# Optimization experiments

Measured on AMD Instinct MI355X. Metric: run time of the kernel, lower is better.

## Reference

```python
import jax, jax.numpy as jnp
import numpy as np

N, E, F_IN, F_HID, K = 100000, 1600000, 64, 64, 6


def setup_inputs() -> dict:
    key = jax.random.key(0)
    k1, k2, k3, k4, k5 = jax.random.split(key, 5)
    x = jax.random.normal(k1, (N, F_IN), dtype=jnp.float32)
    # edges with no self-loops (PyG ChebConv removes self loops before normalization)
    src = jax.random.randint(k2, (E,), 0, N, dtype=jnp.int32)
    off = jax.random.randint(k3, (E,), 1, N, dtype=jnp.int32)
    dst = (src + off) % N
    edge_index = jnp.stack([src, dst], axis=0)
    # Glorot-ish init for the K Chebyshev weight matrices
    W = jax.random.normal(k4, (K, F_IN, F_HID), dtype=jnp.float32) * (1.0 / np.sqrt(F_IN))
    b = jax.random.normal(k5, (F_HID,), dtype=jnp.float32) * 0.01
    return {"x": x, "edge_index": edge_index, "W": W, "b": b}


def reference(x, edge_index, W, b):
    # ChebConv with sym normalization, lambda_max = 2.0 (PyG default):
    # scaled Laplacian L_hat = 2*L/lambda_max - I = -D^{-1/2} A D^{-1/2} (zero diagonal)
    row = edge_index[0].astype(jnp.int32)  # source j
    col = edge_index[1].astype(jnp.int32)  # target i
    n = x.shape[0]
    deg = jax.ops.segment_sum(jnp.ones_like(row, dtype=x.dtype), row, num_segments=n)
    dinv = jnp.where(deg > 0, jax.lax.rsqrt(deg), jnp.zeros_like(deg))
    w = -(dinv[row] * dinv[col])  # [E] edge weights of L_hat

    def prop(h):  # h: [N, F] -> L_hat @ h via gather-scale-scatter
        return jax.ops.segment_sum(w[:, None] * h[row], col, num_segments=n)

    # Chebyshev recurrence: Tx_0 = x, Tx_1 = L_hat x, Tx_k = 2 L_hat Tx_{k-1} - Tx_{k-2}
    Tx0 = x
    out = Tx0 @ W[0]
    Tx1 = prop(Tx0)
    out = out + Tx1 @ W[1]
    for k in range(2, W.shape[0]):
        Tx2 = 2.0 * prop(Tx1) - Tx0
        out = out + Tx2 @ W[k]
        Tx0, Tx1 = Tx1, Tx2
    return jax.nn.relu(out + b)
```

## Files before the change

### kernel.cpp

```cpp
#include <hip/hip_runtime.h>


constexpr int F = 64;
constexpr int SCAN_ELEMS = 2048;
constexpr int BSH = 9;
constexpr int EPB = 2048;
constexpr int PNPW = 8;
constexpr int WFRAG_BLOCKS = 12;

typedef __attribute__((ext_vector_type(8))) short short8;
typedef __attribute__((ext_vector_type(4))) float floatx4;

__device__ __forceinline__ unsigned short f_to_bf(float f) {
    unsigned u = __float_as_uint(f);
    u += 0x7FFFu + ((u >> 16) & 1u);
    return (unsigned short)(u >> 16);
}
__device__ __forceinline__ float bf_to_f(unsigned short s) {
    return __uint_as_float(((unsigned)s) << 16);
}
__device__ __forceinline__ float4 bf4_to_f4(ushort4 u) {
    float4 f;
    f.x = bf_to_f(u.x); f.y = bf_to_f(u.y); f.z = bf_to_f(u.z); f.w = bf_to_f(u.w);
    return f;
}

__global__ void hist2_kernel(const int* __restrict__ row, const int* __restrict__ col,
                             int* __restrict__ gcH, int* __restrict__ gcS,
                             int P, int G, int E) {
    __shared__ int hH[256], hS[256];
    const int tid = threadIdx.x, blk = blockIdx.x;
    hH[tid] = 0; hS[tid] = 0;
    __syncthreads();
    const int start = blk * EPB + tid * 8;
    if (start + 7 < E) {
        const int4 c0 = *(const int4*)(col + start);
        const int4 c1 = *(const int4*)(col + start + 4);
        const int4 r0 = *(const int4*)(row + start);
        const int4 r1 = *(const int4*)(row + start + 4);
        atomicAdd(&hH[c0.x >> BSH], 1); atomicAdd(&hH[c0.y >> BSH], 1);
        atomicAdd(&hH[c0.z >> BSH], 1); atomicAdd(&hH[c0.w >> BSH], 1);
        atomicAdd(&hH[c1.x >> BSH], 1); atomicAdd(&hH[c1.y >> BSH], 1);
        atomicAdd(&hH[c1.z >> BSH], 1); atomicAdd(&hH[c1.w >> BSH], 1);
        atomicAdd(&hS[r0.x >> BSH], 1); atomicAdd(&hS[r0.y >> BSH], 1);
        atomicAdd(&hS[r0.z >> BSH], 1); atomicAdd(&hS[r0.w >> BSH], 1);
        atomicAdd(&hS[r1.x >> BSH], 1); atomicAdd(&hS[r1.y >> BSH], 1);
        atomicAdd(&hS[r1.z >> BSH], 1); atomicAdd(&hS[r1.w >> BSH], 1);
    } else {
        for (int k = start; k < E && k < start + 8; ++k) {
            atomicAdd(&hH[col[k] >> BSH], 1);
            atomicAdd(&hS[row[k] >> BSH], 1);
        }
    }
    __syncthreads();
    if (tid < P) {
        gcH[(size_t)tid * G + blk] = hH[tid];
        gcS[(size_t)tid * G + blk] = hS[tid];
    }
}

__device__ __forceinline__ int4 load_cnt4(const int* __restrict__ cnt, int i, int N) {
    int4 v = make_int4(0, 0, 0, 0);
    if (i + 3 < N) {
        v = *(const int4*)(cnt + i);
    } else {
        if (i + 0 < N) v.x = cnt[i + 0];
        if (i + 1 < N) v.y = cnt[i + 1];
        if (i + 2 < N) v.z = cnt[i + 2];
        if (i + 3 < N) v.w = cnt[i + 3];
    }
    return v;
}

__global__ void scan1_kernel(const int* __restrict__ cnt, int* __restrict__ bsum, int N) {
    const int tid = threadIdx.x;
    const int i = blockIdx.x * SCAN_ELEMS + tid * 8;
    int4 va = load_cnt4(cnt, i, N);
    int4 vb = load_cnt4(cnt, i + 4, N);
    int s = va.x + va.y + va.z + va.w + vb.x + vb.y + vb.z + vb.w;
#pragma unroll
    for (int off = 1; off < 64; off <<= 1) s += __shfl_xor(s, off);
    __shared__ int ws[4];
    if ((tid & 63) == 0) ws[tid >> 6] = s;
    __syncthreads();
    if (tid == 0) bsum[blockIdx.x] = ws[0] + ws[1] + ws[2] + ws[3];
}

__global__ void scan3_kernel(const int* __restrict__ cnt, const int* __restrict__ bsum,
                             int* __restrict__ dst, int N) {
    const int tid = threadIdx.x;
    const int lane = tid & 63, w = tid >> 6;
    const int blk = blockIdx.x;
    __shared__ int wsum[4];
    __shared__ int boffs;
    {
        int a = 0;
        for (int k = tid; k < blk; k += 256) a += bsum[k];
#pragma unroll
        for (int off = 1; off < 64; off <<= 1) a += __shfl_xor(a, off);
        if ((tid & 63) == 0) wsum[tid >> 6] = a;
        __syncthreads();
        if (tid == 0) boffs = wsum[0] + wsum[1] + wsum[2] + wsum[3];
        __syncthreads();
    }
    const int i = blk * SCAN_ELEMS + tid * 8;
    int4 va = load_cnt4(cnt, i, N);
    int4 vb = load_cnt4(cnt, i + 4, N);
    const int s = va.x + va.y + va.z + va.w + vb.x + vb.y + vb.z + vb.w;
    int inc = s;
#pragma unroll
    for (int off = 1; off < 64; off <<= 1) {
        int t = __shfl_up(inc, off);
        if (lane >= off) inc += t;
    }
    __syncthreads();
    if (lane == 63) wsum[w] = inc;
    __syncthreads();
    int wo = 0;
    for (int k = 0; k < w; ++k) wo += wsum[k];
    const int r0 = boffs + wo + inc - s;
    const int r1 = r0 + va.x, r2 = r1 + va.y, r3 = r2 + va.z;
    const int r4 = r3 + va.w, r5 = r4 + vb.x, r6 = r5 + vb.y, r7 = r6 + vb.z;
    if (i + 3 < N) {
        *(int4*)(dst + i) = make_int4(r0, r1, r2, r3);
    } else {
        if (i + 0 < N) dst[i + 0] = r0;
        if (i + 1 < N) dst[i + 1] = r1;
        if (i + 2 < N) dst[i + 2] = r2;
    }
    if (i + 7 < N) {
        *(int4*)(dst + i + 4) = make_int4(r4, r5, r6, r7);
    } else {
        if (i + 4 < N) dst[i + 4] = r4;
        if (i + 5 < N) dst[i + 5] = r5;
        if (i + 6 < N) dst[i + 6] = r6;
    }
}

__global__ void part2_kernel(const int* __restrict__ row, const int* __restrict__ col,
                             const int* __restrict__ goH, const int* __restrict__ goS,
                             int* __restrict__ partH, unsigned short* __restrict__ partS,
                             int P, int G, int E) {
    __shared__ int cH[256], cS[256];
    const int tid = threadIdx.x, blk = blockIdx.x;
    if (tid < P) {
        cH[tid] = goH[(size_t)tid * G + blk];
        cS[tid] = goS[(size_t)tid * G + blk] - E;
    }
    __syncthreads();
    const int start = blk * EPB + tid * 8;
    if (start + 7 < E) {
        const int4 c0 = *(const int4*)(col + start);
        const int4 c1 = *(const int4*)(col + start + 4);
        const int4 r0 = *(const int4*)(row + start);
        const int4 r1 = *(const int4*)(row + start + 4);
#define P2_DO(c, r)                                                    \
        {                                                              \
            const int posH = atomicAdd(&cH[(c) >> BSH], 1);            \
            partH[posH] = (((c) & ((1 << BSH) - 1)) << 23) | (r);      \
            const int posS = atomicAdd(&cS[(r) >> BSH], 1);            \
            partS[posS] = (unsigned short)((r) & ((1 << BSH) - 1));    \
        }
        P2_DO(c0.x, r0.x) P2_DO(c0.y, r0.y) P2_DO(c0.z, r0.z) P2_DO(c0.w, r0.w)
        P2_DO(c1.x, r1.x) P2_DO(c1.y, r1.y) P2_DO(c1.z, r1.z) P2_DO(c1.w, r1.w)
#undef P2_DO
    } else {
        for (int k = start; k < E && k < start + 8; ++k) {
            const int c = col[k], r = row[k];
            const int posH = atomicAdd(&cH[c >> BSH], 1);
            partH[posH] = ((c & ((1 << BSH) - 1)) << 23) | r;
            const int posS = atomicAdd(&cS[r >> BSH], 1);
            partS[posS] = (unsigned short)(r & ((1 << BSH) - 1));
        }
    }
}

__global__ void bucketCDW_kernel(const int* __restrict__ part, const int* __restrict__ goff,
                                 const unsigned short* __restrict__ partS,
                                 const int* __restrict__ goffS,
                                 int* __restrict__ rowptr, int* __restrict__ csr,
                                 float* __restrict__ dinv2, float* __restrict__ rdinv,
                                 const float* __restrict__ x, unsigned short* __restrict__ S0b,
                                 const float* __restrict__ W, unsigned short* __restrict__ Wfrag,
                                 int P, int G, int N, int E) {
    __shared__ int cnt[512];
    __shared__ int excl[512];
    __shared__ int wsum[4];
    const int tid = threadIdx.x;
    const int bb = blockIdx.x;
    if (bb < P) {
        const int b = bb;
        const int base_node = b << BSH;
        const int nn = min(512, N - base_node);
        const int estart = goff[(size_t)b * G];
        const int eend = (b + 1 < P) ? goff[(size_t)(b + 1) * G] : E;

        cnt[tid] = 0; cnt[tid + 256] = 0;
        __syncthreads();
        for (int i = estart + tid; i < eend; i += 256)
            atomicAdd(&cnt[((unsigned)part[i]) >> 23], 1);
        __syncthreads();
        {
            const int lane = tid & 63, w = tid >> 6;
            const int a0 = cnt[2 * tid], a1 = cnt[2 * tid + 1];
            const int ps = a0 + a1;
            int inc = ps;
#pragma unroll
            for (int off = 1; off < 64; off <<= 1) {
                int t = __shfl_up(inc, off);
                if (lane >= off) inc += t;
            }
            if (lane == 63) wsum[w] = inc;
            __syncthreads();
            int wo = 0;
            for (int k = 0; k < w; ++k) wo += wsum[k];
            const int ep = wo + inc - ps;
            excl[2 * tid] = ep;
            excl[2 * tid + 1] = ep + a0;
        }
        __syncthreads();
        for (int ln = tid; ln < nn; ln += 256) rowptr[base_node + ln] = estart + excl[ln];
        if (b == P - 1 && tid == 0) rowptr[N] = E;
        cnt[tid] = 0; cnt[tid + 256] = 0;
        __syncthreads();
        for (int i = estart + tid; i < eend; i += 256) {
            const int pk = part[i];
            const int ln = ((unsigned)pk) >> 23;
            const int pos = atomicAdd(&cnt[ln], 1);
            csr[estart + excl[ln] + pos] = pk & 0x7FFFFF;
        }
    } else if (bb < 2 * P) {
        const int b = bb - P;
        const int base_node = b << BSH;
        const int nn = min(512, N - base_node);
        const int estart = goffS[(size_t)b * G] - E;
        const int eend = ((b + 1 < P) ? goffS[(size_t)(b + 1) * G] - E : E);
        cnt[tid] = 0; cnt[tid + 256] = 0;
        __syncthreads();
        for (int i = estart + tid; i < eend; i += 256)
            atomicAdd(&cnt[partS[i]], 1);
        __syncthreads();
        for (int l = tid; l < nn; l += 256) {
            const int dI = cnt[l];
            const float d = (float)dI;
            const bool ok = dI > 0;
            dinv2[base_node + l] = ok ? 1.0f / d : 0.0f;
            rdinv[base_node + l] = ok ? sqrtf(d) : 0.0f;
        }
        const int ntask = nn * 16;
        for (int t = tid; t < ntask; t += 256) {
            const int l = t >> 4, fq = t & 15;
            const int dI = cnt[l];
            const float dv = dI > 0 ? rsqrtf((float)dI) : 0.0f;
            const size_t off = (size_t)(base_node + l) * F + fq * 4;
            const float4 v = *(const float4*)(x + off);
            ushort4 u;
            u.x = f_to_bf(dv * v.x); u.y = f_to_bf(dv * v.y);
            u.z = f_to_bf(dv * v.z); u.w = f_to_bf(dv * v.w);
            *(ushort4*)(S0b + off) = u;
        }
    } else {
        const int idx = (bb - 2 * P) * 256 + tid;
        if (idx >= 4 * 12 * 64) return;
        const int lane = idx & 63;
        const int s = (idx >> 6) % 12;
        const int ft = idx / (64 * 12);
        const int n = ft * 16 + (lane & 15);
        const int quad = lane >> 4;
        unsigned short v[8];
#pragma unroll
        for (int j = 0; j < 8; ++j) {
            const int kg = s * 32 + quad * 8 + j;
            const int kk = kg >> 6, f = kg & 63;
            v[j] = f_to_bf(W[kk * F * F + f * F + n]);
        }
        ushort4 lo = {v[0], v[1], v[2], v[3]};
        ushort4 hi = {v[4], v[5], v[6], v[7]};
        *(ushort4*)(Wfrag + (size_t)idx * 8) = lo;
        *(ushort4*)(Wfrag + (size_t)idx * 8 + 4) = hi;
    }
}

template <int FIRST>
__global__ __launch_bounds__(256, 6)
void prop_g4(const int* __restrict__ rowptr, const int* __restrict__ csr,
             const float* __restrict__ dinv2, const unsigned short* __restrict__ Sprev,
             const unsigned short* __restrict__ Sm2, unsigned short* __restrict__ Sk, int N) {
    const int lane = threadIdx.x & 63;
    const int g16 = lane & 48;
    const int fl = lane & 15;
    const int wave = threadIdx.x >> 6;
    const int wbase = (blockIdx.x * 4 + wave) * PNPW;
    for (int j = 0; j < PNPW; j += 4) {
        const int n = wbase + j + (g16 >> 4);
        const bool nv = n < N;
        const int nc = nv ? n : N - 1;
        const int s = rowptr[nc], e = rowptr[nc + 1];
        const int len = e - s;
        float4 acc = {0.f, 0.f, 0.f, 0.f};
        for (int c = 0; c < len; c += 16) {
            const int ii = s + c + fl;
            const int idxv = csr[ii < e ? ii : e - 1];
            const int mm = min(16, len - c);
            ushort4 u[16];
#pragma unroll
            for (int t = 0; t < 16; ++t) {
                const int it = __shfl(idxv, g16 + t);
                u[t] = *(const ushort4*)(Sprev + (size_t)it * F + fl * 4);
            }
#pragma unroll
            for (int t = 0; t < 16; ++t) {
                if (t < mm) {
                    const float4 v = bf4_to_f4(u[t]);
                    acc.x += v.x; acc.y += v.y; acc.z += v.z; acc.w += v.w;
                }
            }
        }
        if (nv) {
            const float d2 = dinv2[n];
            float4 sn;
            if (FIRST) {
                sn.x = -d2 * acc.x; sn.y = -d2 * acc.y;
                sn.z = -d2 * acc.z; sn.w = -d2 * acc.w;
            } else {
                const float4 m2 = bf4_to_f4(*(const ushort4*)(Sm2 + (size_t)n * F + fl * 4));
                sn.x = -2.f * d2 * acc.x - m2.x; sn.y = -2.f * d2 * acc.y - m2.y;
                sn.z = -2.f * d2 * acc.z - m2.z; sn.w = -2.f * d2 * acc.w - m2.w;
            }
            ushort4 o;
            o.x = f_to_bf(sn.x); o.y = f_to_bf(sn.y);
            o.z = f_to_bf(sn.z); o.w = f_to_bf(sn.w);
            *(ushort4*)(Sk + (size_t)n * F + fl * 4) = o;
        }
    }
}

__global__ __launch_bounds__(256, 3)
void mfma_out_kernel(const float* __restrict__ x, const unsigned short* __restrict__ Sstack,
                     const unsigned short* __restrict__ Wfrag, const float* __restrict__ rdinv,
                     const float* __restrict__ dinv2, const float* __restrict__ W,
                     const float* __restrict__ b, float* __restrict__ out, int N, int NF) {
    const int lane = threadIdx.x & 63;
    const int wave = threadIdx.x >> 6;
    const int quad = lane >> 4;
    const int fl = lane & 15;
    const int tm = (blockIdx.x * 4 + wave) * 16;
    if (tm >= N) return;
    const int ma = tm + fl;
    const int mac = ma < N ? ma : N - 1;

    const unsigned short* sa = Sstack + (size_t)mac * F + quad * 8;

    short8 Afr[12];
#pragma unroll
    for (int s = 0; s < 12; ++s) {
        const int kk = s >> 1, f0 = (s & 1) * 32;
        Afr[s] = __builtin_nontemporal_load((const short8*)(sa + (size_t)kk * NF + f0));
    }

    floatx4 C0 = {0.f, 0.f, 0.f, 0.f};
    floatx4 C1 = {0.f, 0.f, 0.f, 0.f};
    floatx4 C2 = {0.f, 0.f, 0.f, 0.f};
    floatx4 C3 = {0.f, 0.f, 0.f, 0.f};
    const unsigned short* wf = Wfrag + (size_t)lane * 8;
#pragma unroll
    for (int s = 0; s < 12; ++s) {
        const short8 B0 = *(const short8*)(wf + (size_t)(0 * 12 + s) * 64 * 8);
        const short8 B1 = *(const short8*)(wf + (size_t)(1 * 12 + s) * 64 * 8);
        const short8 B2 = *(const short8*)(wf + (size_t)(2 * 12 + s) * 64 * 8);
        const short8 B3 = *(const short8*)(wf + (size_t)(3 * 12 + s) * 64 * 8);
        C0 = __builtin_amdgcn_mfma_f32_16x16x32_bf16(Afr[s], B0, C0, 0, 0, 0);
        C1 = __builtin_amdgcn_mfma_f32_16x16x32_bf16(Afr[s], B1, C1, 0, 0, 0);
        C2 = __builtin_amdgcn_mfma_f32_16x16x32_bf16(Afr[s], B2, C2, 0, 0, 0);
        C3 = __builtin_amdgcn_mfma_f32_16x16x32_bf16(Afr[s], B3, C3, 0, 0, 0);
    }

    const float bl0 = b[0 * 16 + fl];
    const float bl1 = b[1 * 16 + fl];
    const float bl2 = b[2 * 16 + fl];
    const float bl3 = b[3 * 16 + fl];

#pragma unroll
    for (int r = 0; r < 4; ++r) {
        const int m = tm + quad * 4 + r;
        if (m >= N) continue;
        const float rs = rdinv[m];
        const bool z = (dinv2[m] == 0.0f);
        float v0 = rs * C0[r], v1 = rs * C1[r], v2 = rs * C2[r], v3 = rs * C3[r];
        if (z) {
            const float* xr = x + (size_t)m * F;
            float f0 = 0.f, f1 = 0.f, f2 = 0.f, f3 = 0.f;
            for (int f = 0; f < F; ++f) {
                const float xv = xr[f];
                const float* w0 = W + 0 * F * F + f * F;
                const float* w2 = W + 2 * F * F + f * F;
                const float* w4 = W + 4 * F * F + f * F;
                f0 += xv * (w0[0 * 16 + fl] - w2[0 * 16 + fl] + w4[0 * 16 + fl]);
                f1 += xv * (w0[1 * 16 + fl] - w2[1 * 16 + fl] + w4[1 * 16 + fl]);
                f2 += xv * (w0[2 * 16 + fl] - w2[2 * 16 + fl] + w4[2 * 16 + fl]);
                f3 += xv * (w0[3 * 16 + fl] - w2[3 * 16 + fl] + w4[3 * 16 + fl]);
            }
            v0 = f0; v1 = f1; v2 = f2; v3 = f3;
        }
        float* orow = out + (size_t)m * F;
        __builtin_nontemporal_store(fmaxf(v0 + bl0, 0.f), orow + 0 * 16 + fl);
        __builtin_nontemporal_store(fmaxf(v1 + bl1, 0.f), orow + 1 * 16 + fl);
        __builtin_nontemporal_store(fmaxf(v2 + bl2, 0.f), orow + 2 * 16 + fl);
        __builtin_nontemporal_store(fmaxf(v3 + bl3, 0.f), orow + 3 * 16 + fl);
    }
}

extern "C" void kernel_launch(void* const* d_in, const int* in_sizes, int n_in,
                              void* d_out, int out_size, void* d_ws, size_t ws_size,
                              hipStream_t stream) {
    const float* x = (const float*)d_in[0];
    const int* ei = (const int*)d_in[1];
    const float* W = (const float*)d_in[2];
    const float* b = (const float*)d_in[3];

    const int N = in_sizes[0] / F;
    const int E = in_sizes[1] / 2;
    const int NF = N * F;
    const int* row = ei;
    const int* col = ei + E;

    const int P = (N + 511) >> BSH;
    const int G = (E + EPB - 1) / EPB;
    const int M = P * G;
    const int M2 = 2 * M;

    char* p = (char*)d_ws;
    auto alloc = [&](size_t bytes) {
        char* r = p;
        p += (bytes + 63) & ~(size_t)63;
        return r;
    };
    float* dinv2  = (float*)alloc((size_t)N * sizeof(float));
    float* rdinv  = (float*)alloc((size_t)N * sizeof(float));
    int*   rowptr = (int*)alloc((size_t)(N + 1) * sizeof(int));
    int*   bsum   = (int*)alloc(256 * sizeof(int));
    int*   gc     = (int*)alloc((size_t)M2 * sizeof(int));
    int*   go     = (int*)alloc((size_t)M2 * sizeof(int));
    int*   csr    = (int*)alloc((size_t)E * sizeof(int));
    unsigned short* Sstack = (unsigned short*)alloc((size_t)6 * NF * sizeof(unsigned short));
    unsigned short* Wfrag  = (unsigned short*)alloc((size_t)4 * 12 * 64 * 8 * sizeof(unsigned short));
    int* partH = (int*)(Sstack + (size_t)4 * NF);
    unsigned short* partS = Sstack + (size_t)5 * NF;
    float* out = (float*)d_out;
    (void)ws_size;

    const int B = 256;
    const int nsb = (M2 + SCAN_ELEMS - 1) / SCAN_ELEMS;
    const int pgrid = (N + 4 * PNPW - 1) / (4 * PNPW);

    hist2_kernel<<<G, B, 0, stream>>>(row, col, gc, gc + M, P, G, E);
    scan1_kernel<<<nsb, B, 0, stream>>>(gc, bsum, M2);
    scan3_kernel<<<nsb, B, 0, stream>>>(gc, bsum, go, M2);
    part2_kernel<<<G, B, 0, stream>>>(row, col, go, go + M, partH, partS, P, G, E);
    bucketCDW_kernel<<<2 * P + WFRAG_BLOCKS, B, 0, stream>>>(
        partH, go, partS, go + M, rowptr, csr, dinv2, rdinv, x, Sstack, W, Wfrag,
        P, G, N, E);

    unsigned short* S1 = Sstack + (size_t)1 * NF;
    unsigned short* S2 = Sstack + (size_t)2 * NF;
    unsigned short* S3 = Sstack + (size_t)3 * NF;
    unsigned short* S4 = Sstack + (size_t)4 * NF;
    unsigned short* S5 = Sstack + (size_t)5 * NF;
    prop_g4<1><<<pgrid, B, 0, stream>>>(rowptr, csr, dinv2, Sstack, Sstack, S1, N);
    prop_g4<0><<<pgrid, B, 0, stream>>>(rowptr, csr, dinv2, S1, Sstack, S2, N);
    prop_g4<0><<<pgrid, B, 0, stream>>>(rowptr, csr, dinv2, S2, S1, S3, N);
    prop_g4<0><<<pgrid, B, 0, stream>>>(rowptr, csr, dinv2, S3, S2, S4, N);
    prop_g4<0><<<pgrid, B, 0, stream>>>(rowptr, csr, dinv2, S4, S3, S5, N);
    mfma_out_kernel<<<(N + 63) / 64, 256, 0, stream>>>(x, Sstack, Wfrag, rdinv, dinv2,
                                                       W, b, out, N, NF);
}
```

Before: 419.0 us.

## Split S0/Wfrag init into separate wide kernel and raise prop occupancy

Moves the x·dinv to bf16 S0 conversion and the W fragment packing out of the bucket/degree kernel into a new kernel that runs over the whole feature array. The old version did that conversion in only P (~196) blocks, a serial tail inside bucket construction. A new dinv array carries the degree scale between the kernels. Since S0 is written after bucketing, the partition scratch now aliases the S0/S1 buffers instead of S4/S5. It also raises prop_g4 launch bounds from 6 to 8 blocks per CU, which may cost registers or cause spills.

New measurement: 493.0 us. 17.7% more time.

```diff
diff --git a/kernel.cpp b/kernel.cpp
--- a/kernel.cpp
+++ b/kernel.cpp
@@ -175,14 +175,13 @@
     }
 }
 
-__global__ void bucketCDW_kernel(const int* __restrict__ part, const int* __restrict__ goff,
-                                 const unsigned short* __restrict__ partS,
-                                 const int* __restrict__ goffS,
-                                 int* __restrict__ rowptr, int* __restrict__ csr,
-                                 float* __restrict__ dinv2, float* __restrict__ rdinv,
-                                 const float* __restrict__ x, unsigned short* __restrict__ S0b,
-                                 const float* __restrict__ W, unsigned short* __restrict__ Wfrag,
-                                 int P, int G, int N, int E) {
+__global__ void bucketCD_kernel(const int* __restrict__ part, const int* __restrict__ goff,
+                                const unsigned short* __restrict__ partS,
+                                const int* __restrict__ goffS,
+                                int* __restrict__ rowptr, int* __restrict__ csr,
+                                float* __restrict__ dinv, float* __restrict__ dinv2,
+                                float* __restrict__ rdinv,
+                                int P, int G, int N, int E) {
     __shared__ int cnt[512];
     __shared__ int excl[512];
     __shared__ int wsum[4];
@@ -229,7 +228,7 @@
             const int pos = atomicAdd(&cnt[ln], 1);
             csr[estart + excl[ln] + pos] = pk & 0x7FFFFF;
         }
-    } else if (bb < 2 * P) {
+    } else {
         const int b = bb - P;
         const int base_node = b << BSH;
         const int nn = min(512, N - base_node);
@@ -244,23 +243,20 @@
             const int dI = cnt[l];
             const float d = (float)dI;
             const bool ok = dI > 0;
+            dinv[base_node + l]  = ok ? rsqrtf(d) : 0.0f;
             dinv2[base_node + l] = ok ? 1.0f / d : 0.0f;
             rdinv[base_node + l] = ok ? sqrtf(d) : 0.0f;
         }
-        const int ntask = nn * 16;
-        for (int t = tid; t < ntask; t += 256) {
-            const int l = t >> 4, fq = t & 15;
-            const int dI = cnt[l];
-            const float dv = dI > 0 ? rsqrtf((float)dI) : 0.0f;
-            const size_t off = (size_t)(base_node + l) * F + fq * 4;
-            const float4 v = *(const float4*)(x + off);
-            ushort4 u;
-            u.x = f_to_bf(dv * v.x); u.y = f_to_bf(dv * v.y);
-            u.z = f_to_bf(dv * v.z); u.w = f_to_bf(dv * v.w);
-            *(ushort4*)(S0b + off) = u;
-        }
-    } else {
-        const int idx = (bb - 2 * P) * 256 + tid;
+    }
+}
+
+__global__ void init_ws0_kernel(const float* __restrict__ W, unsigned short* __restrict__ Wfrag,
+                                const float* __restrict__ dinv, const float* __restrict__ x,
+                                unsigned short* __restrict__ S0b, int NF) {
+    const int tid = threadIdx.x;
+    const int bid = blockIdx.x;
+    if (bid < WFRAG_BLOCKS) {
+        const int idx = bid * 256 + tid;
         if (idx >= 4 * 12 * 64) return;
         const int lane = idx & 63;
         const int s = (idx >> 6) % 12;
@@ -278,11 +274,21 @@
         ushort4 hi = {v[4], v[5], v[6], v[7]};
         *(ushort4*)(Wfrag + (size_t)idx * 8) = lo;
         *(ushort4*)(Wfrag + (size_t)idx * 8 + 4) = hi;
+    } else {
+        const int i = (bid - WFRAG_BLOCKS) * 256 + tid;
+        const int j = i * 4;
+        if (j >= NF) return;
+        const float dv = dinv[j >> 6];
+        const float4 v = *(const float4*)(x + j);
+        ushort4 u;
+        u.x = f_to_bf(dv * v.x); u.y = f_to_bf(dv * v.y);
+        u.z = f_to_bf(dv * v.z); u.w = f_to_bf(dv * v.w);
+        *(ushort4*)(S0b + j) = u;
     }
 }
 
 template <int FIRST>
-__global__ __launch_bounds__(256, 6)
+__global__ __launch_bounds__(256, 8)
 void prop_g4(const int* __restrict__ rowptr, const int* __restrict__ csr,
              const float* __restrict__ dinv2, const unsigned short* __restrict__ Sprev,
              const unsigned short* __restrict__ Sm2, unsigned short* __restrict__ Sk, int N) {
@@ -435,6 +441,7 @@
         p += (bytes + 63) & ~(size_t)63;
         return r;
     };
+    float* dinv   = (float*)alloc((size_t)N * sizeof(float));
     float* dinv2  = (float*)alloc((size_t)N * sizeof(float));
     float* rdinv  = (float*)alloc((size_t)N * sizeof(float));
     int*   rowptr = (int*)alloc((size_t)(N + 1) * sizeof(int));
@@ -444,22 +451,23 @@
     int*   csr    = (int*)alloc((size_t)E * sizeof(int));
     unsigned short* Sstack = (unsigned short*)alloc((size_t)6 * NF * sizeof(unsigned short));
     unsigned short* Wfrag  = (unsigned short*)alloc((size_t)4 * 12 * 64 * 8 * sizeof(unsigned short));
-    int* partH = (int*)(Sstack + (size_t)4 * NF);
-    unsigned short* partS = Sstack + (size_t)5 * NF;
+    int* partH = (int*)Sstack;
+    unsigned short* partS = Sstack + (size_t)NF;
     float* out = (float*)d_out;
     (void)ws_size;
 
     const int B = 256;
     const int nsb = (M2 + SCAN_ELEMS - 1) / SCAN_ELEMS;
     const int pgrid = (N + 4 * PNPW - 1) / (4 * PNPW);
+    const int igrid = WFRAG_BLOCKS + (NF / 4 + B - 1) / B;
 
     hist2_kernel<<<G, B, 0, stream>>>(row, col, gc, gc + M, P, G, E);
     scan1_kernel<<<nsb, B, 0, stream>>>(gc, bsum, M2);
     scan3_kernel<<<nsb, B, 0, stream>>>(gc, bsum, go, M2);
     part2_kernel<<<G, B, 0, stream>>>(row, col, go, go + M, partH, partS, P, G, E);
-    bucketCDW_kernel<<<2 * P + WFRAG_BLOCKS, B, 0, stream>>>(
-        partH, go, partS, go + M, rowptr, csr, dinv2, rdinv, x, Sstack, W, Wfrag,
-        P, G, N, E);
+    bucketCD_kernel<<<2 * P, B, 0, stream>>>(partH, go, partS, go + M, rowptr, csr,
+                                             dinv, dinv2, rdinv, P, G, N, E);
+    init_ws0_kernel<<<igrid, B, 0, stream>>>(W, Wfrag, dinv, x, Sstack, NF);
 
     unsigned short* S1 = Sstack + (size_t)1 * NF;
     unsigned short* S2 = Sstack + (size_t)2 * NF;
```
